# Kernel optimization log

Measured on AMD Instinct MI355X. Metric: run time of the kernel, lower is better.

## Reference

```python
import jax, jax.numpy as jnp
import numpy as np

D_MODEL = 1024
D_STATE = 32
EXPAND = 2
D_INNER = D_MODEL * EXPAND
B_SZ = 2
SEQ = 512


def setup_inputs() -> dict:
    key = jax.random.key(0)
    ks = jax.random.split(key, 10)
    x = jax.random.normal(ks[0], (B_SZ, SEQ, D_MODEL), dtype=jnp.float32)
    W_in = jax.random.normal(ks[1], (2 * D_INNER, D_MODEL), dtype=jnp.float32) * 0.02
    A_log = jax.random.uniform(ks[2], (D_INNER, D_STATE), minval=-4.0, maxval=-1.0, dtype=jnp.float32)
    W_B = jax.random.normal(ks[3], (D_STATE, D_MODEL), dtype=jnp.float32) * 0.02
    W_C = jax.random.normal(ks[4], (D_STATE, D_MODEL), dtype=jnp.float32) * 0.02
    W_dt = jax.random.normal(ks[5], (D_INNER, D_MODEL), dtype=jnp.float32) * 0.02
    b_dt = jnp.zeros((D_INNER,), dtype=jnp.float32)
    dt_bias = jnp.zeros((D_INNER,), dtype=jnp.float32) - 4.0
    rope_freq = jax.random.normal(ks[6], (D_STATE // 2,), dtype=jnp.float32) * 0.01
    ln_w = jnp.ones((D_INNER,), dtype=jnp.float32)
    ln_b = jnp.zeros((D_INNER,), dtype=jnp.float32)
    W_out = jax.random.normal(ks[7], (D_MODEL, D_INNER), dtype=jnp.float32) * 0.02
    return {"x": x, "W_in": W_in, "A_log": A_log, "W_B": W_B, "W_C": W_C,
            "W_dt": W_dt, "b_dt": b_dt, "dt_bias": dt_bias, "rope_freq": rope_freq,
            "ln_w": ln_w, "ln_b": ln_b, "W_out": W_out}


def _forward(x, W_in, A_log, W_B, W_C, W_dt, b_dt, dt_bias, rope_freq, ln_w, ln_b, W_out):
    B, L, _ = x.shape
    half = D_STATE // 2
    offset = 0

    xz = jnp.einsum('bld,ed->ble', x, W_in)                 # [B,L,2*D_INNER]
    x_inner = xz[..., :D_INNER]                             # [B,L,DI]
    z = jax.nn.silu(xz[..., D_INNER:])                      # [B,L,DI]

    A = -jnp.exp(A_log)                                     # [DI,DS]
    Bm = jnp.einsum('bld,nd->bln', x, W_B)                  # [B,L,DS]
    Cm = jnp.einsum('bld,nd->bln', x, W_C)                  # [B,L,DS]
    dt = jax.nn.softplus(jnp.einsum('bld,ed->ble', x, W_dt) + b_dt + dt_bias)  # [B,L,DI]

    # trapezoidal discretization
    dtA = dt[..., None] * A                                 # [B,L,DI,DS]
    denom = 1.0 - dtA / 2.0
    A_bar = (1.0 + dtA / 2.0) / denom                       # [B,L,DI,DS]
    B_bar = dt[..., None] / denom                           # [B,L,DI,DS]

    # per-step rope rotation angles: angle_t = rope_freq * (t + offset)
    t_idx = jnp.arange(L, dtype=jnp.float32) + offset       # [L]
    ang = t_idx[:, None] * rope_freq                        # [L,half]
    cos_a = jnp.cos(ang)
    sin_a = jnp.sin(ang)

    def step(state, inp):
        A_t, Bb_t, B_t, x_t, C_t, c_t, s_t = inp
        # state update: [B,DI,DS]
        state = A_t * state + Bb_t * B_t[:, None, :] * x_t[:, :, None]
        real = state[..., :half]
        imag = state[..., half:]
        state = jnp.concatenate([real * c_t - imag * s_t,
                                 real * s_t + imag * c_t], axis=-1)
        y_t = jnp.einsum('bds,bs->bd', state, C_t)          # [B,DI]
        return state, y_t

    state0 = jnp.zeros((B, D_INNER, D_STATE), dtype=x.dtype)
    xs = (jnp.swapaxes(A_bar, 0, 1), jnp.swapaxes(B_bar, 0, 1),
          jnp.swapaxes(Bm, 0, 1), jnp.swapaxes(x_inner, 0, 1),
          jnp.swapaxes(Cm, 0, 1), cos_a, sin_a)
    final_state, ys = jax.lax.scan(step, state0, xs)        # ys: [L,B,DI]
    out = jnp.swapaxes(ys, 0, 1) * z                        # [B,L,DI]

    # LayerNorm over last dim (eps=1e-5, torch default)
    mu = jnp.mean(out, axis=-1, keepdims=True)
    var = jnp.mean((out - mu) ** 2, axis=-1, keepdims=True)
    out = (out - mu) * jax.lax.rsqrt(var + 1e-5) * ln_w + ln_b

    out = jnp.einsum('ble,de->bld', out, W_out)             # [B,L,D_MODEL]
    return out, final_state


def reference(x, W_in, A_log, W_B, W_C, W_dt, b_dt, dt_bias, rope_freq, ln_w, ln_b, W_out):
    return _forward(x, W_in, A_log, W_B, W_C, W_dt, b_dt, dt_bias, rope_freq, ln_w, ln_b, W_out)
```

## Files before the change

### kernel.cpp

```cpp
#include <hip/hip_runtime.h>
#include <math.h>

#define B_SZ 2
#define SEQ 512
#define DM 1024
#define DI 2048
#define DS 32
#define TOK (B_SZ*SEQ)
#define NCH 8
#define CLEN (SEQ/NCH)
#define NPAIRH 32768

#define NFUSED 6272

typedef float v2f __attribute__((ext_vector_type(2)));

__device__ __forceinline__ unsigned short f2bf(float f) {
  unsigned int u = __builtin_bit_cast(unsigned int, f);
  unsigned int r = u + 0x7fffu + ((u >> 16) & 1u);
  return (unsigned short)(r >> 16);
}

template<int CTRL>
__device__ __forceinline__ float row_ror_add(float x) {
  int s = __builtin_amdgcn_update_dpp(0, __builtin_bit_cast(int, x), CTRL, 0xf, 0xf, false);
  return x + __builtin_bit_cast(float, s);
}
__device__ __forceinline__ float row16_sum(float v) {
  v = row_ror_add<0x121>(v);
  v = row_ror_add<0x122>(v);
  v = row_ror_add<0x124>(v);
  v = row_ror_add<0x128>(v);
  return v;
}

__global__ __launch_bounds__(256) void fused_cast(const float* __restrict__ x,
                                                  const float* __restrict__ W_in,
                                                  const float* __restrict__ W_dt,
                                                  const float* __restrict__ W_B,
                                                  const float* __restrict__ W_C,
                                                  const float* __restrict__ W_out,
                                                  unsigned short* __restrict__ xb,
                                                  unsigned short* __restrict__ wcat,
                                                  unsigned short* __restrict__ wob) {
  int g = blockIdx.x * 256 + threadIdx.x;
  const float* s; unsigned short* dd; int off;
  if      (g <  131072) { s = x;     dd = xb;             off = 0; }
  else if (g <  655360) { s = W_in;  dd = wcat;           off = 131072; }
  else if (g <  917504) { s = W_dt;  dd = wcat + 4194304; off = 655360; }
  else if (g <  921600) { s = W_B;   dd = wcat + 6291456; off = 917504; }
  else if (g <  925696) { s = W_C;   dd = wcat + 6324224; off = 921600; }
  else if (g < 1187840) { s = W_out; dd = wob;            off = 925696; }
  else return;
  int i = g - off;
  float4 a = ((const float4*)s)[i * 2];
  float4 b = ((const float4*)s)[i * 2 + 1];
  union { unsigned short us[8]; uint4 v; } o;
  o.us[0] = f2bf(a.x); o.us[1] = f2bf(a.y); o.us[2] = f2bf(a.z); o.us[3] = f2bf(a.w);
  o.us[4] = f2bf(b.x); o.us[5] = f2bf(b.y); o.us[6] = f2bf(b.z); o.us[7] = f2bf(b.w);
  ((uint4*)dd)[i] = o.v;
}

typedef __attribute__((ext_vector_type(8))) short  frag8;
typedef __attribute__((ext_vector_type(4))) float  facc4;

__device__ __forceinline__ void gload_lds16(const unsigned short* g, unsigned short* l) {
  __builtin_amdgcn_global_load_lds((const __attribute__((address_space(1))) unsigned int*)g,
                                   (__attribute__((address_space(3))) unsigned int*)l, 16, 0, 0);
}
__device__ __forceinline__ void gload_lds16f(const float* g, float* l) {
  __builtin_amdgcn_global_load_lds((const __attribute__((address_space(1))) unsigned int*)g,
                                   (__attribute__((address_space(3))) unsigned int*)l, 16, 0, 0);
}

__device__ __forceinline__ float softplus_fast(float v) {
  return fmaxf(v, 0.f) + __logf(1.f + __expf(-fabsf(v)));
}

template<int MT, int NT, int KSP, bool ROUTE>
__global__ __launch_bounds__(256) void gemm_mfma(const unsigned short* __restrict__ A,
                                                 const unsigned short* __restrict__ Bw,
                                                 int K,
                                                 float* __restrict__ o_xs,
                                                 float* __restrict__ o_zb,
                                                 float* __restrict__ o_dts,
                                                 float* __restrict__ o_bcb,
                                                 const float* __restrict__ b_dt,
                                                 const float* __restrict__ dt_bias,
                                                 float* __restrict__ o_c, int ldc) {
  __shared__ __align__(16) unsigned short As[64 * 64];
  __shared__ __align__(16) unsigned short Bs[64 * 64];
  const int tid = threadIdx.x;
  const int w = tid >> 6, lane = tid & 63;
  const int wm = w >> 1, wn = w & 1;
  const int bid = blockIdx.x;
  const int Wk = (bid & 7) * ((int)gridDim.x >> 3) + (bid >> 3);
  const int ks = Wk / (MT * NT);
  const int rem = Wk % (MT * NT);
  const int m0 = (rem % MT) * 64;
  const int n0 = (rem / MT) * 64;
  const int kLen = K / KSP, kBeg = ks * kLen;
  const int r = lane & 15, q = lane >> 4;
  const int srow = lane >> 3;
  const int scol = ((lane & 7) ^ (srow & 7)) * 8;
  facc4 acc[2][2] = {};
  const unsigned short* Ag = A + (size_t)m0 * K + kBeg;
  const unsigned short* Bg = Bw + (size_t)n0 * K + kBeg;

  for (int k0 = 0; k0 < kLen; k0 += 64) {
#pragma unroll
    for (int k = 0; k < 2; ++k) {
      int ch = w * 2 + k;
      gload_lds16(Ag + (size_t)(ch * 8 + srow) * K + k0 + scol, &As[ch * 512]);
      gload_lds16(Bg + (size_t)(ch * 8 + srow) * K + k0 + scol, &Bs[ch * 512]);
    }
    __syncthreads();
#pragma unroll
    for (int kk = 0; kk < 2; ++kk) {
      frag8 af[2], bf[2];
      const int sw = ((kk * 4 + q) ^ (r & 7)) * 8;
#pragma unroll
      for (int i = 0; i < 2; ++i)
        af[i] = *(const frag8*)&As[(wm * 32 + i * 16 + r) * 64 + sw];
#pragma unroll
      for (int jj = 0; jj < 2; ++jj)
        bf[jj] = *(const frag8*)&Bs[(wn * 32 + jj * 16 + r) * 64 + sw];
#pragma unroll
      for (int i = 0; i < 2; ++i)
#pragma unroll
        for (int jj = 0; jj < 2; ++jj)
          acc[i][jj] = __builtin_amdgcn_mfma_f32_16x16x32_bf16(af[i], bf[jj], acc[i][jj], 0, 0, 0);
    }
    __syncthreads();
  }

#pragma unroll
  for (int i = 0; i < 2; ++i) {
#pragma unroll
    for (int jj = 0; jj < 2; ++jj) {
      int n = n0 + wn * 32 + jj * 16 + r;
      int mb = m0 + wm * 32 + i * 16 + q * 4;
      if (ROUTE) {
        if (n < 2048) {
#pragma unroll
          for (int rg = 0; rg < 4; ++rg)
            o_xs[(size_t)(mb + rg) * DI + n] = acc[i][jj][rg];
        } else if (n < 4096) {
#pragma unroll
          for (int rg = 0; rg < 4; ++rg)
            o_zb[(size_t)(mb + rg) * DI + (n - 2048)] = acc[i][jj][rg];
        } else if (n < 6144) {
          int d = n - 4096;
          float bias = b_dt[d] + dt_bias[d];
#pragma unroll
          for (int rg = 0; rg < 4; ++rg)
            o_dts[(size_t)(mb + rg) * DI + d] = softplus_fast(acc[i][jj][rg] + bias);
        } else if (n < 6176) {
#pragma unroll
          for (int rg = 0; rg < 4; ++rg)
            o_bcb[(size_t)(mb + rg) * DS + (n - 6144)] = acc[i][jj][rg];
        } else if (n < 6208) {
#pragma unroll
          for (int rg = 0; rg < 4; ++rg)
            o_bcb[(size_t)TOK * DS + (size_t)(mb + rg) * DS + (n - 6176)] = acc[i][jj][rg];
        }
      } else {
        float* oc = o_c + (size_t)ks * (MT * 64) * ldc;
#pragma unroll
        for (int rg = 0; rg < 4; ++rg)
          oc[(size_t)(mb + rg) * ldc + n] = acc[i][jj][rg];
      }
    }
  }
}

__global__ __launch_bounds__(256) void addk(const float* __restrict__ p0,
                                            const float* __restrict__ p1,
                                            float* __restrict__ o) {
  int i = blockIdx.x * 256 + threadIdx.x;
  float4 a = ((const float4*)p0)[i];
  float4 b = ((const float4*)p1)[i];
  ((float4*)o)[i] = make_float4(a.x + b.x, a.y + b.y, a.z + b.z, a.w + b.w);
}

__global__ __launch_bounds__(256) void scan_p1(const float* __restrict__ xs,
                                               const float* __restrict__ dts,
                                               const float* __restrict__ bcb,
                                               const float* __restrict__ A_log,
                                               const float* __restrict__ rope,
                                               float* __restrict__ Pbuf) {
  __shared__ __align__(16) float lds[6144];
  const int blk = blockIdx.x;
  const int c = blk >> 7;
  const int sub = blk & 127;
  const int b = sub >> 6;
  const int dbase = (sub & 63) << 5;
  const int tid = threadIdx.x;
  const int wv = tid >> 6, lane = tid & 63;
  const int j = tid & 15;
  const int ca = (tid >> 4) & 15;
  const int l0 = c * CLEN;
  const size_t base = (size_t)(b * SEQ + l0);

  {
    int row = wv * 16 + (lane >> 3);
    int col = (lane & 7) << 2;
#pragma unroll
    for (int k = 0; k < 2; ++k) {
      gload_lds16f(xs  + (base + row + k * 8) * DI + dbase + col, &lds[(wv * 16 + k * 8) * 32]);
      gload_lds16f(dts + (base + row + k * 8) * DI + dbase + col, &lds[2048 + (wv * 16 + k * 8) * 32]);
    }
#pragma unroll
    for (int k = 0; k < 2; ++k) {
      int seg = wv * 2 + k;
      gload_lds16f(bcb + base * DS + seg * 256 + lane * 4, &lds[4096 + seg * 256]);
    }
  }

  const int dA = dbase + 2 * ca;
  v2f Ar, Ai;
  Ar.x = -0.5f * expf(A_log[dA * DS + j]);
  Ar.y = -0.5f * expf(A_log[(dA + 1) * DS + j]);
  Ai.x = -0.5f * expf(A_log[dA * DS + j + 16]);
  Ai.y = -0.5f * expf(A_log[(dA + 1) * DS + j + 16]);
  const float fr = rope[j];
  float sn, cs, sF, cF;
  sincosf((float)l0 * fr, &sn, &cs);
  sincosf(fr, &sF, &cF);
  __syncthreads();

  v2f p00 = {1.f, 1.f}, p01 = {0.f, 0.f}, p10 = {0.f, 0.f}, p11 = {1.f, 1.f};
  v2f ur = {0.f, 0.f}, ui = {0.f, 0.f};

#pragma unroll 4
  for (int tt = 0; tt < CLEN; ++tt) {
    const int ro = tt * 32;
    v2f xin = *(const v2f*)&lds[ro + 2 * ca];
    v2f dtd = *(const v2f*)&lds[2048 + ro + 2 * ca];
    float Br = lds[4096 + ro + j];
    float Bi = lds[4096 + ro + j + 16];
    v2f hr = dtd * Ar, hi = dtd * Ai;
    v2f invr, invi;
    invr.x = __builtin_amdgcn_rcpf(1.f - hr.x);
    invr.y = __builtin_amdgcn_rcpf(1.f - hr.y);
    invi.x = __builtin_amdgcn_rcpf(1.f - hi.x);
    invi.y = __builtin_amdgcn_rcpf(1.f - hi.y);
    v2f Abr = 2.f * invr - 1.f;
    v2f Abi = 2.f * invi - 1.f;
    v2f dx = dtd * xin;
    v2f bxr = dx * invr * Br;
    v2f bxi = dx * invi * Bi;
    v2f tr = Abr * ur + bxr;
    v2f ti = Abi * ui + bxi;
    ur = tr * cs - ti * sn;
    ui = tr * sn + ti * cs;
    v2f q00 = Abr * p00, q01 = Abr * p01;
    v2f q10 = Abi * p10, q11 = Abi * p11;
    p00 = q00 * cs - q10 * sn; p10 = q00 * sn + q10 * cs;
    p01 = q01 * cs - q11 * sn; p11 = q01 * sn + q11 * cs;
    float nc = fmaf(cs, cF, -sn * sF);
    float ns = fmaf(sn, cF,  cs * sF);
    cs = nc; sn = ns;
  }
  const int pc = (b * 1024 + (dbase >> 1) + ca) * 16 + j;
  float2* Pb2 = (float2*)Pbuf;
  Pb2[(c * 6 + 0) * NPAIRH + pc] = make_float2(p00.x, p00.y);
  Pb2[(c * 6 + 1) * NPAIRH + pc] = make_float2(p01.x, p01.y);
  Pb2[(c * 6 + 2) * NPAIRH + pc] = make_float2(p10.x, p10.y);
  Pb2[(c * 6 + 3) * NPAIRH + pc] = make_float2(p11.x, p11.y);
  Pb2[(c * 6 + 4) * NPAIRH + pc] = make_float2(ur.x, ur.y);
  Pb2[(c * 6 + 5) * NPAIRH + pc] = make_float2(ui.x, ui.y);
}

__global__ __launch_bounds__(256) void scan_p3(const float* __restrict__ xs,
                                               const float* __restrict__ dts,
                                               const float* __restrict__ bcb,
                                               const float* __restrict__ A_log,
                                               const float* __restrict__ rope,
                                               const float* __restrict__ Pbuf,
                                               float* __restrict__ y,
                                               float* __restrict__ fstate) {
  __shared__ __align__(16) float lds[8192];
  const int blk = blockIdx.x;
  const int c = blk >> 7;
  const int sub = blk & 127;
  const int b = sub >> 6;
  const int dbase = (sub & 63) << 5;
  const int tid = threadIdx.x;
  const int wv = tid >> 6, lane = tid & 63;
  const int j = tid & 15;
  const int ca = (tid >> 4) & 15;
  const int l0 = c * CLEN;
  const size_t base = (size_t)(b * SEQ + l0);

  {
    int row = wv * 16 + (lane >> 3);
    int col = (lane & 7) << 2;
#pragma unroll
    for (int k = 0; k < 2; ++k) {
      gload_lds16f(xs  + (base + row + k * 8) * DI + dbase + col, &lds[(wv * 16 + k * 8) * 32]);
      gload_lds16f(dts + (base + row + k * 8) * DI + dbase + col, &lds[2048 + (wv * 16 + k * 8) * 32]);
    }
#pragma unroll
    for (int k = 0; k < 2; ++k) {
      int seg = wv * 2 + k;
      gload_lds16f(bcb + base * DS + seg * 256 + lane * 4, &lds[4096 + seg * 256]);
      gload_lds16f(bcb + (size_t)TOK * DS + base * DS + seg * 256 + lane * 4, &lds[6144 + seg * 256]);
    }
  }

  const int dA = dbase + 2 * ca;
  v2f Ar, Ai;
  Ar.x = -0.5f * expf(A_log[dA * DS + j]);
  Ar.y = -0.5f * expf(A_log[(dA + 1) * DS + j]);
  Ai.x = -0.5f * expf(A_log[dA * DS + j + 16]);
  Ai.y = -0.5f * expf(A_log[(dA + 1) * DS + j + 16]);
  const float fr = rope[j];
  float sn, cs, sF, cF;
  sincosf((float)l0 * fr, &sn, &cs);
  sincosf(fr, &sF, &cF);

  const int pc = (b * 1024 + (dbase >> 1) + ca) * 16 + j;
  const float2* Pb2 = (const float2*)Pbuf;
  v2f sr = {0.f, 0.f}, si = {0.f, 0.f};
  for (int k = 0; k < c; ++k) {
    float2 f;
    f = Pb2[(k * 6 + 0) * NPAIRH + pc]; v2f p00 = {f.x, f.y};
    f = Pb2[(k * 6 + 1) * NPAIRH + pc]; v2f p01 = {f.x, f.y};
    f = Pb2[(k * 6 + 2) * NPAIRH + pc]; v2f p10 = {f.x, f.y};
    f = Pb2[(k * 6 + 3) * NPAIRH + pc]; v2f p11 = {f.x, f.y};
    f = Pb2[(k * 6 + 4) * NPAIRH + pc]; v2f ur  = {f.x, f.y};
    f = Pb2[(k * 6 + 5) * NPAIRH + pc]; v2f ui  = {f.x, f.y};
    v2f nr = p00 * sr + p01 * si + ur;
    v2f ni = p10 * sr + p11 * si + ui;
    sr = nr; si = ni;
  }
  __syncthreads();

  float* yp = y + base * DI + dA;

#pragma unroll 4
  for (int tt = 0; tt < CLEN; ++tt) {
    const int ro = tt * 32;
    v2f xin = *(const v2f*)&lds[ro + 2 * ca];
    v2f dtd = *(const v2f*)&lds[2048 + ro + 2 * ca];
    float Br = lds[4096 + ro + j];
    float Bi = lds[4096 + ro + j + 16];
    float Cr = lds[6144 + ro + j];
    float Ci = lds[6144 + ro + j + 16];
    v2f hr = dtd * Ar, hi = dtd * Ai;
    v2f invr, invi;
    invr.x = __builtin_amdgcn_rcpf(1.f - hr.x);
    invr.y = __builtin_amdgcn_rcpf(1.f - hr.y);
    invi.x = __builtin_amdgcn_rcpf(1.f - hi.x);
    invi.y = __builtin_amdgcn_rcpf(1.f - hi.y);
    v2f Abr = 2.f * invr - 1.f;
    v2f Abi = 2.f * invi - 1.f;
    v2f dx = dtd * xin;
    v2f bxr = dx * invr * Br;
    v2f bxi = dx * invi * Bi;
    v2f tr = Abr * sr + bxr;
    v2f ti = Abi * si + bxi;
    sr = tr * cs - ti * sn;
    si = tr * sn + ti * cs;
    v2f p = sr * Cr + si * Ci;
    float pA = row16_sum(p.x);
    float pB = row16_sum(p.y);
    if (j == 0) *(float2*)&yp[tt * DI] = make_float2(pA, pB);
    float nc = fmaf(cs, cF, -sn * sF);
    float ns = fmaf(sn, cF,  cs * sF);
    cs = nc; sn = ns;
  }
  if (c == NCH - 1) {
    fstate[((size_t)b * DI + dA) * DS + j]          = sr.x;
    fstate[((size_t)b * DI + dA) * DS + j + 16]     = si.x;
    fstate[((size_t)b * DI + dA + 1) * DS + j]      = sr.y;
    fstate[((size_t)b * DI + dA + 1) * DS + j + 16] = si.y;
  }
}

__global__ __launch_bounds__(256) void gate_ln(const float* __restrict__ y,
                                               const float* __restrict__ zb,
                                               const float* __restrict__ lw,
                                               const float* __restrict__ lb,
                                               unsigned short* __restrict__ o) {
  int tok = blockIdx.x;
  int t = threadIdx.x;
  float g[8];
  float sum = 0.f, sq = 0.f;
#pragma unroll
  for (int i = 0; i < 8; ++i) {
    int dd = t + i * 256;
    float yv = y[(size_t)tok * DI + dd];
    float zv = zb[(size_t)tok * DI + dd];
    float sg = zv / (1.f + __expf(-zv));
    float v = yv * sg;
    g[i] = v; sum += v; sq += v * v;
  }
#pragma unroll
  for (int off = 32; off; off >>= 1) { sum += __shfl_xor(sum, off); sq += __shfl_xor(sq, off); }
  __shared__ float rs[4], rq[4];
  int w = t >> 6;
  if ((t & 63) == 0) { rs[w] = sum; rq[w] = sq; }
  __syncthreads();
  sum = rs[0] + rs[1] + rs[2] + rs[3];
  sq  = rq[0] + rq[1] + rq[2] + rq[3];
  float mu = sum * (1.f / DI);
  float var = sq * (1.f / DI) - mu * mu;
  float rstd = rsqrtf(var + 1e-5f);
#pragma unroll
  for (int i = 0; i < 8; ++i) {
    int dd = t + i * 256;
    o[(size_t)tok * DI + dd] = f2bf((g[i] - mu) * rstd * lw[dd] + lb[dd]);
  }
}

extern "C" void kernel_launch(void* const* d_in, const int* in_sizes, int n_in,
                              void* d_out, int out_size, void* d_ws, size_t ws_size,
                              hipStream_t stream) {
  const float* x       = (const float*)d_in[0];
  const float* W_in    = (const float*)d_in[1];
  const float* A_log   = (const float*)d_in[2];
  const float* W_B     = (const float*)d_in[3];
  const float* W_C     = (const float*)d_in[4];
  const float* W_dt    = (const float*)d_in[5];
  const float* b_dt    = (const float*)d_in[6];
  const float* dt_bias = (const float*)d_in[7];
  const float* rope    = (const float*)d_in[8];
  const float* ln_w    = (const float*)d_in[9];
  const float* ln_b    = (const float*)d_in[10];
  const float* W_out   = (const float*)d_in[11];
  float* out = (float*)d_out;
  float* ws = (float*)d_ws;

  float* xs   = ws;
  float* zb   = ws + 2097152;
  float* dts  = ws + 4194304;
  float* bcb  = ws + 6291456;
  unsigned short* wob  = (unsigned short*)(ws + 6356992);
  unsigned short* xb   = (unsigned short*)(ws + 7405568);
  unsigned short* wcat = (unsigned short*)(ws + 7929856);
  float* Pbuf = ws + 7929856;
  float* yb   = ws + 11141120;
  unsigned short* lnb = (unsigned short*)(ws + 13238272);
  float* Pk   = ws;
  float* fstate = out + (size_t)TOK * DM;

  fused_cast<<<4640, 256, 0, stream>>>(x, W_in, W_dt, W_B, W_C, W_out, xb, wcat, wob);
  gemm_mfma<16, 98, 1, true><<<16 * 98, 256, 0, stream>>>(
      xb, wcat, DM, xs, zb, dts, bcb, b_dt, dt_bias, nullptr, 0);
  scan_p1<<<(NCH - 1) * 128, 256, 0, stream>>>(xs, dts, bcb, A_log, rope, Pbuf);
  scan_p3<<<NCH * 128, 256, 0, stream>>>(xs, dts, bcb, A_log, rope, Pbuf, yb, fstate);
  gate_ln<<<TOK, 256, 0, stream>>>(yb, zb, ln_w, ln_b, lnb);
  gemm_mfma<16, 16, 2, false><<<16 * 16 * 2, 256, 0, stream>>>(
      lnb, wob, DI, nullptr, nullptr, nullptr, nullptr, nullptr, nullptr, Pk, DM);
  addk<<<(TOK * DM) / 1024, 256, 0, stream>>>(Pk, Pk + (size_t)TOK * DM, out);
}
```

Baseline: 205.0 us.

## Use 128x64 tiles with block swizzle for the input projection GEMM

Replaces the generic 64x64-tile MFMA GEMM for the fused input projection with a dedicated kernel that uses 128-row by 64-column tiles. Each wave now computes a 4x2 grid of 16x16 MFMA accumulators. Block indices are remapped so that consecutive blocks share the same weight column tile across M tiles, which should improve L2 reuse. The larger tile halves the block count and raises register use per thread, which may lower occupancy.

```diff
diff --git a/kernel.cpp b/kernel.cpp
--- a/kernel.cpp
+++ b/kernel.cpp
@@ -75,6 +75,95 @@
 
 __device__ __forceinline__ float softplus_fast(float v) {
   return fmaxf(v, 0.f) + __logf(1.f + __expf(-fabsf(v)));
+}
+
+__global__ __launch_bounds__(256) void gemm1_big(const unsigned short* __restrict__ A,
+                                                 const unsigned short* __restrict__ Bw,
+                                                 float* __restrict__ o_xs,
+                                                 float* __restrict__ o_zb,
+                                                 float* __restrict__ o_dts,
+                                                 float* __restrict__ o_bcb,
+                                                 const float* __restrict__ b_dt,
+                                                 const float* __restrict__ dt_bias) {
+  __shared__ __align__(16) unsigned short As[128 * 64];
+  __shared__ __align__(16) unsigned short Bs[64 * 64];
+  const int K = DM;
+  const int tid = threadIdx.x;
+  const int w = tid >> 6, lane = tid & 63;
+  const int wm = w >> 1, wn = w & 1;
+  const int bid = blockIdx.x;
+  const int Wk = (bid & 7) * 98 + (bid >> 3);
+  const int m0 = (Wk & 7) * 128;
+  const int n0 = (Wk >> 3) * 64;
+  const int r = lane & 15, q = lane >> 4;
+  const int srow = lane >> 3;
+  const int scol = ((lane & 7) ^ srow) * 8;
+  facc4 acc[4][2] = {};
+  const unsigned short* Ag = A + (size_t)m0 * K;
+  const unsigned short* Bg = Bw + (size_t)n0 * K;
+
+  for (int k0 = 0; k0 < DM; k0 += 64) {
+#pragma unroll
+    for (int k = 0; k < 4; ++k) {
+      int ch = w * 4 + k;
+      gload_lds16(Ag + (size_t)(ch * 8 + srow) * K + k0 + scol, &As[ch * 512]);
+    }
+#pragma unroll
+    for (int k = 0; k < 2; ++k) {
+      int ch = w * 2 + k;
+      gload_lds16(Bg + (size_t)(ch * 8 + srow) * K + k0 + scol, &Bs[ch * 512]);
+    }
+    __syncthreads();
+#pragma unroll
+    for (int kk = 0; kk < 2; ++kk) {
+      frag8 af[4], bfr[2];
+      const int sw = ((kk * 4 + q) ^ (r & 7)) * 8;
+#pragma unroll
+      for (int i = 0; i < 4; ++i)
+        af[i] = *(const frag8*)&As[(wm * 64 + i * 16 + r) * 64 + sw];
+#pragma unroll
+      for (int jj = 0; jj < 2; ++jj)
+        bfr[jj] = *(const frag8*)&Bs[(wn * 32 + jj * 16 + r) * 64 + sw];
+#pragma unroll
+      for (int i = 0; i < 4; ++i)
+#pragma unroll
+        for (int jj = 0; jj < 2; ++jj)
+          acc[i][jj] = __builtin_amdgcn_mfma_f32_16x16x32_bf16(af[i], bfr[jj], acc[i][jj], 0, 0, 0);
+    }
+    __syncthreads();
+  }
+
+#pragma unroll
+  for (int i = 0; i < 4; ++i) {
+#pragma unroll
+    for (int jj = 0; jj < 2; ++jj) {
+      int n = n0 + wn * 32 + jj * 16 + r;
+      int mb = m0 + wm * 64 + i * 16 + q * 4;
+      if (n < 2048) {
+#pragma unroll
+        for (int rg = 0; rg < 4; ++rg)
+          o_xs[(size_t)(mb + rg) * DI + n] = acc[i][jj][rg];
+      } else if (n < 4096) {
+#pragma unroll
+        for (int rg = 0; rg < 4; ++rg)
+          o_zb[(size_t)(mb + rg) * DI + (n - 2048)] = acc[i][jj][rg];
+      } else if (n < 6144) {
+        int d = n - 4096;
+        float bias = b_dt[d] + dt_bias[d];
+#pragma unroll
+        for (int rg = 0; rg < 4; ++rg)
+          o_dts[(size_t)(mb + rg) * DI + d] = softplus_fast(acc[i][jj][rg] + bias);
+      } else if (n < 6176) {
+#pragma unroll
+        for (int rg = 0; rg < 4; ++rg)
+          o_bcb[(size_t)(mb + rg) * DS + (n - 6144)] = acc[i][jj][rg];
+      } else if (n < 6208) {
+#pragma unroll
+        for (int rg = 0; rg < 4; ++rg)
+          o_bcb[(size_t)TOK * DS + (size_t)(mb + rg) * DS + (n - 6176)] = acc[i][jj][rg];
+      }
+    }
+  }
 }
 
 template<int MT, int NT, int KSP, bool ROUTE>
@@ -447,8 +536,7 @@
   float* fstate = out + (size_t)TOK * DM;
 
   fused_cast<<<4640, 256, 0, stream>>>(x, W_in, W_dt, W_B, W_C, W_out, xb, wcat, wob);
-  gemm_mfma<16, 98, 1, true><<<16 * 98, 256, 0, stream>>>(
-      xb, wcat, DM, xs, zb, dts, bcb, b_dt, dt_bias, nullptr, 0);
+  gemm1_big<<<784, 256, 0, stream>>>(xb, wcat, xs, zb, dts, bcb, b_dt, dt_bias);
   scan_p1<<<(NCH - 1) * 128, 256, 0, stream>>>(xs, dts, bcb, A_log, rope, Pbuf);
   scan_p3<<<NCH * 128, 256, 0, stream>>>(xs, dts, bcb, A_log, rope, Pbuf, yb, fstate);
   gate_ln<<<TOK, 256, 0, stream>>>(yb, zb, ln_w, ln_b, lnb);
```

New measurement: 204.0 us. No clear change (-0.5%).
